# Kernel optimization log

Measured on AMD Instinct MI355X. Metric: run time of the kernel, lower is better.

Reference implementation:

```python
import jax, jax.numpy as jnp
import numpy as np

EPS = 1e-05
GROUPS = 8


def setup_inputs() -> dict:
    key = jax.random.key(0)
    k1, k2, k3 = jax.random.split(key, 3)
    N, C, H, W = 32, 256, 56, 56
    x = jax.random.normal(k1, (N, C, H, W), dtype=jnp.float32)
    weight = jnp.ones((C,), dtype=jnp.float32)
    bias = jnp.zeros((C,), dtype=jnp.float32)
    gate_logits = jnp.array([2.8, 0.2, 1.1], dtype=jnp.float32)
    diag_proj = jnp.array([[0.08, -0.05, 0.08],
                           [-0.03, 0.08, -0.01],
                           [-0.05, -0.04, -0.07]], dtype=jnp.float32)
    return {"x": x, "weight": weight, "bias": bias,
            "gate_logits": gate_logits, "diag_proj": diag_proj}


def reference(x, weight, bias, gate_logits, diag_proj):
    xf = x.astype(jnp.float32)
    N, C, H, W = xf.shape

    # variance descriptor (differentiable: first-instance path recomputes without detach)
    batch_var = jnp.var(xf, axis=(0, 2, 3)).mean()    # per-channel var -> mean
    sample_var = jnp.var(xf, axis=(1, 2, 3)).mean()   # per-sample var -> mean
    channel_var = jnp.var(xf, axis=1).mean()          # var over channels at each (n,h,w) -> mean
    desc = jnp.tanh(jnp.log(jnp.maximum(jnp.stack([batch_var, sample_var, channel_var]), EPS)))

    gate = jax.nn.softmax(gate_logits + diag_proj @ desc)  # [3]

    # batch norm (training mode: batch statistics over N,H,W per channel)
    mu_b = xf.mean(axis=(0, 2, 3), keepdims=True)
    var_b = xf.var(axis=(0, 2, 3), keepdims=True)
    x_bn = (xf - mu_b) / jnp.sqrt(var_b + EPS)

    # layer norm = group_norm with 1 group: per-sample stats over C,H,W
    mu_l = xf.mean(axis=(1, 2, 3), keepdims=True)
    var_l = xf.var(axis=(1, 2, 3), keepdims=True)
    x_ln = (xf - mu_l) / jnp.sqrt(var_l + EPS)

    # group norm with GROUPS groups
    xg = xf.reshape(N, GROUPS, C // GROUPS, H, W)
    mu_g = xg.mean(axis=(2, 3, 4), keepdims=True)
    var_g = xg.var(axis=(2, 3, 4), keepdims=True)
    x_gn = ((xg - mu_g) / jnp.sqrt(var_g + EPS)).reshape(N, C, H, W)

    mixed = gate[0] * x_bn + gate[1] * x_ln + gate[2] * x_gn
    y = mixed * weight[None, :, None, None] + bias[None, :, None, None]
    return y.astype(x.dtype)
```

## Files before the change

kernel.cpp:

```cpp
#include <hip/hip_runtime.h>
#include <hip/hip_bf16.h>

#define NN 32
#define CC 256
#define HW 3136
#define HW4 784
#define CHW 802816
#define CHW4 200704
#define NCHW 25690112
#define GROUPS 8
#define CPG 32
#define NHW 100352
#define GHW 100352
#define EPSF 1e-5f

#define PB16 49
#define NSTAT (NN*PB16)
#define NPT2 NSTAT

typedef float f32x4 __attribute__((ext_vector_type(4)));

__global__ __launch_bounds__(256) void stats_kernel(
    const float4* __restrict__ x4,
    float2* __restrict__ S12p,
    float* __restrict__ pT2)
{
    const int bx = blockIdx.x;
    const int n = bx / PB16, pb = bx - n * PB16;
    const int tid = threadIdx.x;
    const int w = tid >> 6, lane = tid & 63;
    const int cl = lane >> 3;
    const int pl = lane & 7;
    const int P0 = pb * 16;

    const float4* base = x4 + (size_t)n * CHW4 + P0 + pl;

    __shared__ float2 shS[256][9];
    __shared__ float4 shT[4][16];

    float s1a[8], s2a[8];
    float4 T0 = make_float4(0.f, 0.f, 0.f, 0.f);
    float4 T1 = make_float4(0.f, 0.f, 0.f, 0.f);
    #pragma unroll
    for (int k = 0; k < 8; ++k) {
        const int c = (k * 4 + w) * 8 + cl;
        float4 v0 = base[(size_t)c * HW4];
        float4 v1 = base[(size_t)c * HW4 + 8];
        T0.x += v0.x; T0.y += v0.y; T0.z += v0.z; T0.w += v0.w;
        T1.x += v1.x; T1.y += v1.y; T1.z += v1.z; T1.w += v1.w;
        s1a[k] = v0.x + v0.y + v0.z + v0.w + v1.x + v1.y + v1.z + v1.w;
        s2a[k] = v0.x*v0.x + v0.y*v0.y + v0.z*v0.z + v0.w*v0.w
               + v1.x*v1.x + v1.y*v1.y + v1.z*v1.z + v1.w*v1.w;
    }

    #pragma unroll
    for (int k = 0; k < 8; ++k) {
        const int c = (k * 4 + w) * 8 + cl;
        shS[c][pl] = make_float2(s1a[k], s2a[k]);
    }
    __syncthreads();

    {
        float a = 0.f, b = 0.f;
        #pragma unroll
        for (int j = 0; j < 8; ++j) {
            float2 v = shS[tid][j];
            a += v.x; b += v.y;
        }
        S12p[(size_t)bx * 256 + tid] = make_float2(a, b);
    }

    #pragma unroll
    for (int off = 8; off < 64; off <<= 1) {
        T0.x += __shfl_xor(T0.x, off, 64);
        T0.y += __shfl_xor(T0.y, off, 64);
        T0.z += __shfl_xor(T0.z, off, 64);
        T0.w += __shfl_xor(T0.w, off, 64);
        T1.x += __shfl_xor(T1.x, off, 64);
        T1.y += __shfl_xor(T1.y, off, 64);
        T1.z += __shfl_xor(T1.z, off, 64);
        T1.w += __shfl_xor(T1.w, off, 64);
    }
    if (lane < 8) {
        shT[w][pl] = T0;
        shT[w][8 + pl] = T1;
    }
    __syncthreads();
    if (tid < 16) {
        float4 a = shT[0][tid], b = shT[1][tid], c4 = shT[2][tid], d = shT[3][tid];
        const float tx = a.x + b.x + c4.x + d.x;
        const float ty = a.y + b.y + c4.y + d.y;
        const float tz = a.z + b.z + c4.z + d.z;
        const float tw = a.w + b.w + c4.w + d.w;
        float t2 = tx*tx + ty*ty + tz*tz + tw*tw;
        #pragma unroll
        for (int off = 1; off < 16; off <<= 1) t2 += __shfl_down(t2, off, 64);
        if (tid == 0) pT2[bx] = t2;
    }
}

__global__ __launch_bounds__(256) void fold_kernel(
    const float2* __restrict__ S12p, float2* __restrict__ S12)
{
    const int n = blockIdx.x, c = threadIdx.x;
    const float2* p = S12p + (size_t)n * PB16 * 256 + c;
    float a = 0.f, b = 0.f;
    #pragma unroll 7
    for (int pb = 0; pb < PB16; ++pb) {
        float2 v = p[(size_t)pb * 256];
        a += v.x; b += v.y;
    }
    S12[n * 256 + c] = make_float2(a, b);
}

__global__ __launch_bounds__(256) void finalize_kernel(
    const float2* __restrict__ S12, const float* __restrict__ partialT2,
    const float* __restrict__ gate_logits, const float* __restrict__ diag_proj,
    float2* __restrict__ CB, float2* __restrict__ CL, float2* __restrict__ CG,
    float* __restrict__ GT)
{
    const int tid = threadIdx.x;
    __shared__ float sh_red1[4], sh_red2[4], sh_red3[4], sh_red4[4];

    const float inv_NHW  = 1.f / (float)NHW;
    const float inv_CHW  = 1.f / (float)CHW;
    const float inv_GHW  = 1.f / (float)GHW;
    const float inv_NCHW = 1.f / (float)NCHW;

    const int c = tid;
    float s1 = 0.f, s2 = 0.f;
    for (int n = 0; n < NN; ++n) {
        float2 v = S12[n * CC + c];
        s1 += v.x; s2 += v.y;
    }
    const float mu_b  = s1 * inv_NHW;
    const float var_b = s2 * inv_NHW - mu_b * mu_b;
    CB[c] = make_float2(mu_b, rsqrtf(var_b + EPSF));

    const int ng_n = tid >> 3, ng_g = tid & 7;
    float s1g = 0.f, s2g = 0.f;
    for (int cc2 = 0; cc2 < CPG; ++cc2) {
        float2 v = S12[ng_n * CC + ng_g * CPG + cc2];
        s1g += v.x; s2g += v.y;
    }
    const float mu_g  = s1g * inv_GHW;
    const float var_g = s2g * inv_GHW - mu_g * mu_g;
    CG[tid] = make_float2(mu_g, rsqrtf(var_g + EPSF));

    float s1l = s1g, s2l = s2g;
    #pragma unroll
    for (int off = 1; off < 8; off <<= 1) {
        s1l += __shfl_xor(s1l, off, 64);
        s2l += __shfl_xor(s2l, off, 64);
    }
    float var_l_contrib = 0.f;
    if (ng_g == 0) {
        const float mu_l  = s1l * inv_CHW;
        const float var_l = s2l * inv_CHW - mu_l * mu_l;
        CL[ng_n] = make_float2(mu_l, rsqrtf(var_l + EPSF));
        var_l_contrib = var_l;
    }

    float t2p = 0.f;
    for (int i = tid; i < NPT2; i += 256) t2p += partialT2[i];

    float r1 = var_b, r2 = s2, r3 = var_l_contrib, r4 = t2p;
    #pragma unroll
    for (int off = 32; off; off >>= 1) {
        r1 += __shfl_down(r1, off, 64);
        r2 += __shfl_down(r2, off, 64);
        r3 += __shfl_down(r3, off, 64);
        r4 += __shfl_down(r4, off, 64);
    }
    const int wave = tid >> 6, lane = tid & 63;
    if (lane == 0) { sh_red1[wave] = r1; sh_red2[wave] = r2; sh_red3[wave] = r3; sh_red4[wave] = r4; }
    __syncthreads();
    if (tid == 0) {
        const float sum_var_b = sh_red1[0] + sh_red1[1] + sh_red1[2] + sh_red1[3];
        const float total_x2  = sh_red2[0] + sh_red2[1] + sh_red2[2] + sh_red2[3];
        const float sum_var_l = sh_red3[0] + sh_red3[1] + sh_red3[2] + sh_red3[3];
        const float sum_T2    = sh_red4[0] + sh_red4[1] + sh_red4[2] + sh_red4[3];

        const float batch_var   = sum_var_b * (1.f / (float)CC);
        const float sample_var  = sum_var_l * (1.f / (float)NN);
        const float channel_var = total_x2 * inv_NCHW
                                - sum_T2 * inv_NHW * (1.f / ((float)CC * (float)CC));

        float desc[3];
        desc[0] = tanhf(logf(fmaxf(batch_var,   EPSF)));
        desc[1] = tanhf(logf(fmaxf(sample_var,  EPSF)));
        desc[2] = tanhf(logf(fmaxf(channel_var, EPSF)));

        float lg[3];
        #pragma unroll
        for (int i = 0; i < 3; ++i) {
            lg[i] = gate_logits[i] + diag_proj[i*3+0]*desc[0]
                                   + diag_proj[i*3+1]*desc[1]
                                   + diag_proj[i*3+2]*desc[2];
        }
        const float m = fmaxf(lg[0], fmaxf(lg[1], lg[2]));
        const float e0 = expf(lg[0]-m), e1 = expf(lg[1]-m), e2 = expf(lg[2]-m);
        const float inv = 1.f / (e0 + e1 + e2);
        GT[0] = e0 * inv; GT[1] = e1 * inv; GT[2] = e2 * inv;
    }
}

__global__ __launch_bounds__(256) void apply_kernel(
    const f32x4* __restrict__ x4,
    const float* __restrict__ weight, const float* __restrict__ bias,
    const float2* __restrict__ CB, const float2* __restrict__ CL,
    const float2* __restrict__ CG, const float* __restrict__ GT,
    f32x4* __restrict__ y4)
{
    const int nc = blockIdx.x;
    const int n = nc >> 8, ch = nc & 255, g = ch >> 5;
    const float g0 = GT[0], g1 = GT[1], g2 = GT[2];
    const float2 cb = CB[ch], cl2 = CL[n], cg2 = CG[n * 8 + g];
    const float w = weight[ch], bi = bias[ch];
    const float scale = g0 * cb.y + g1 * cl2.y + g2 * cg2.y;
    const float offs  = g0 * cb.x * cb.y + g1 * cl2.x * cl2.y + g2 * cg2.x * cg2.y;
    const float a = w * scale;
    const float b = fmaf(-w, offs, bi);

    const f32x4* xp = x4 + (size_t)nc * HW4;
    f32x4* yp = y4 + (size_t)nc * HW4;
    const int tid = threadIdx.x;

    f32x4 v0 = xp[tid];
    f32x4 v1 = xp[tid + 256];
    f32x4 v2 = xp[tid + 512];
    f32x4 v3;
    if (tid < 16) v3 = xp[tid + 768];

    f32x4 r0, r1, r2, r3;
    r0.x = fmaf(v0.x, a, b); r0.y = fmaf(v0.y, a, b); r0.z = fmaf(v0.z, a, b); r0.w = fmaf(v0.w, a, b);
    r1.x = fmaf(v1.x, a, b); r1.y = fmaf(v1.y, a, b); r1.z = fmaf(v1.z, a, b); r1.w = fmaf(v1.w, a, b);
    r2.x = fmaf(v2.x, a, b); r2.y = fmaf(v2.y, a, b); r2.z = fmaf(v2.z, a, b); r2.w = fmaf(v2.w, a, b);
    __builtin_nontemporal_store(r0, &yp[tid]);
    __builtin_nontemporal_store(r1, &yp[tid + 256]);
    __builtin_nontemporal_store(r2, &yp[tid + 512]);
    if (tid < 16) {
        r3.x = fmaf(v3.x, a, b); r3.y = fmaf(v3.y, a, b); r3.z = fmaf(v3.z, a, b); r3.w = fmaf(v3.w, a, b);
        __builtin_nontemporal_store(r3, &yp[tid + 768]);
    }
}

extern "C" void kernel_launch(void* const* d_in, const int* in_sizes, int n_in,
                              void* d_out, int out_size, void* d_ws, size_t ws_size,
                              hipStream_t stream) {
    const float* x           = (const float*)d_in[0];
    const float* weight      = (const float*)d_in[1];
    const float* bias        = (const float*)d_in[2];
    const float* gate_logits = (const float*)d_in[3];
    const float* diag_proj   = (const float*)d_in[4];
    float* out = (float*)d_out;

    float* ws   = (float*)d_ws;
    float2* S12p = (float2*)ws;
    float2* S12  = (float2*)(ws + 802816);
    float2* CB   = (float2*)(ws + 819200);
    float2* CL   = (float2*)(ws + 819712);
    float2* CG   = (float2*)(ws + 819776);
    float*  GT   = ws + 820288;
    float*  pT2  = ws + 820296;

    stats_kernel<<<NSTAT, 256, 0, stream>>>((const float4*)x, S12p, pT2);
    fold_kernel<<<NN, 256, 0, stream>>>(S12p, S12);
    finalize_kernel<<<1, 256, 0, stream>>>(S12, pT2, gate_logits, diag_proj,
                                           CB, CL, CG, GT);
    apply_kernel<<<NN * CC, 256, 0, stream>>>((const f32x4*)x, weight, bias,
                                              CB, CL, CG, GT, (f32x4*)out);
}
```

Baseline: 62.97 us.

## Restructure stats pass into wide-pixel windows split across channel quarters

The stats kernel now gives each block a 64-float4 pixel window (13 windows per sample) and a quarter of the channels, instead of 16-pixel slices covering all channels. Each wavefront reads contiguous 1 KB rows per channel, and the per-channel partial sums are cut by about 4x, which shrinks the fold work and workspace. The cost is padded, predicated loads in the last window, more shared memory per block, and an extra cross-block partial for the channel-variance term. The apply kernel also switches from nontemporal stores to ordinary stores.

```diff
diff --git a/kernel.cpp b/kernel.cpp
--- a/kernel.cpp
+++ b/kernel.cpp
@@ -3,9 +3,7 @@
 
 #define NN 32
 #define CC 256
-#define HW 3136
 #define HW4 784
-#define CHW 802816
 #define CHW4 200704
 #define NCHW 25690112
 #define GROUPS 8
@@ -14,8 +12,8 @@
 #define GHW 100352
 #define EPSF 1e-5f
 
-#define PB16 49
-#define NSTAT (NN*PB16)
+#define WIN 13
+#define NSTAT (NN*WIN*4)
 #define NPT2 NSTAT
 
 typedef float f32x4 __attribute__((ext_vector_type(4)));
@@ -26,75 +24,59 @@
     float* __restrict__ pT2)
 {
     const int bx = blockIdx.x;
-    const int n = bx / PB16, pb = bx - n * PB16;
+    const int q   = bx & 3;
+    const int nw  = bx >> 2;
+    const int win = nw % WIN;
+    const int n   = nw / WIN;
     const int tid = threadIdx.x;
-    const int w = tid >> 6, lane = tid & 63;
-    const int cl = lane >> 3;
-    const int pl = lane & 7;
-    const int P0 = pb * 16;
-
-    const float4* base = x4 + (size_t)n * CHW4 + P0 + pl;
-
-    __shared__ float2 shS[256][9];
-    __shared__ float4 shT[4][16];
-
-    float s1a[8], s2a[8];
-    float4 T0 = make_float4(0.f, 0.f, 0.f, 0.f);
-    float4 T1 = make_float4(0.f, 0.f, 0.f, 0.f);
-    #pragma unroll
-    for (int k = 0; k < 8; ++k) {
-        const int c = (k * 4 + w) * 8 + cl;
-        float4 v0 = base[(size_t)c * HW4];
-        float4 v1 = base[(size_t)c * HW4 + 8];
-        T0.x += v0.x; T0.y += v0.y; T0.z += v0.z; T0.w += v0.w;
-        T1.x += v1.x; T1.y += v1.y; T1.z += v1.z; T1.w += v1.w;
-        s1a[k] = v0.x + v0.y + v0.z + v0.w + v1.x + v1.y + v1.z + v1.w;
-        s2a[k] = v0.x*v0.x + v0.y*v0.y + v0.z*v0.z + v0.w*v0.w
-               + v1.x*v1.x + v1.y*v1.y + v1.z*v1.z + v1.w*v1.w;
-    }
-
-    #pragma unroll
-    for (int k = 0; k < 8; ++k) {
-        const int c = (k * 4 + w) * 8 + cl;
-        shS[c][pl] = make_float2(s1a[k], s2a[k]);
-    }
+    const int w   = tid >> 6, lane = tid & 63;
+
+    const int p4 = win * 64 + lane;
+    const bool pv = p4 < HW4;
+    const int c0 = q * 64 + w * 16;
+
+    const float4* base = x4 + (size_t)n * CHW4 + p4;
+
+    __shared__ float sh1[64][65];
+    __shared__ float sh2[64][65];
+    __shared__ float4 shT[4][64];
+
+    float4 T = make_float4(0.f, 0.f, 0.f, 0.f);
+    #pragma unroll
+    for (int k = 0; k < 16; ++k) {
+        const int c = c0 + k;
+        float4 v = make_float4(0.f, 0.f, 0.f, 0.f);
+        if (pv) v = base[(size_t)c * HW4];
+        T.x += v.x; T.y += v.y; T.z += v.z; T.w += v.w;
+        sh1[w * 16 + k][lane] = v.x + v.y + v.z + v.w;
+        sh2[w * 16 + k][lane] = v.x*v.x + v.y*v.y + v.z*v.z + v.w*v.w;
+    }
+    shT[w][lane] = T;
     __syncthreads();
 
     {
+        const int cl = tid >> 2, seg = tid & 3;
         float a = 0.f, b = 0.f;
         #pragma unroll
-        for (int j = 0; j < 8; ++j) {
-            float2 v = shS[tid][j];
-            a += v.x; b += v.y;
+        for (int j = 0; j < 16; ++j) {
+            a += sh1[cl][seg * 16 + j];
+            b += sh2[cl][seg * 16 + j];
         }
-        S12p[(size_t)bx * 256 + tid] = make_float2(a, b);
-    }
-
-    #pragma unroll
-    for (int off = 8; off < 64; off <<= 1) {
-        T0.x += __shfl_xor(T0.x, off, 64);
-        T0.y += __shfl_xor(T0.y, off, 64);
-        T0.z += __shfl_xor(T0.z, off, 64);
-        T0.w += __shfl_xor(T0.w, off, 64);
-        T1.x += __shfl_xor(T1.x, off, 64);
-        T1.y += __shfl_xor(T1.y, off, 64);
-        T1.z += __shfl_xor(T1.z, off, 64);
-        T1.w += __shfl_xor(T1.w, off, 64);
-    }
-    if (lane < 8) {
-        shT[w][pl] = T0;
-        shT[w][8 + pl] = T1;
-    }
-    __syncthreads();
-    if (tid < 16) {
-        float4 a = shT[0][tid], b = shT[1][tid], c4 = shT[2][tid], d = shT[3][tid];
-        const float tx = a.x + b.x + c4.x + d.x;
-        const float ty = a.y + b.y + c4.y + d.y;
-        const float tz = a.z + b.z + c4.z + d.z;
-        const float tw = a.w + b.w + c4.w + d.w;
+        a += __shfl_down(a, 1, 64); b += __shfl_down(b, 1, 64);
+        a += __shfl_down(a, 2, 64); b += __shfl_down(b, 2, 64);
+        if (seg == 0)
+            S12p[(size_t)(n * WIN + win) * 256 + q * 64 + cl] = make_float2(a, b);
+    }
+
+    if (tid < 64) {
+        float4 a0 = shT[0][tid], a1 = shT[1][tid], a2 = shT[2][tid], a3 = shT[3][tid];
+        const float tx = a0.x + a1.x + a2.x + a3.x;
+        const float ty = a0.y + a1.y + a2.y + a3.y;
+        const float tz = a0.z + a1.z + a2.z + a3.z;
+        const float tw = a0.w + a1.w + a2.w + a3.w;
         float t2 = tx*tx + ty*ty + tz*tz + tw*tw;
         #pragma unroll
-        for (int off = 1; off < 16; off <<= 1) t2 += __shfl_down(t2, off, 64);
+        for (int off = 32; off; off >>= 1) t2 += __shfl_down(t2, off, 64);
         if (tid == 0) pT2[bx] = t2;
     }
 }
@@ -103,11 +85,11 @@
     const float2* __restrict__ S12p, float2* __restrict__ S12)
 {
     const int n = blockIdx.x, c = threadIdx.x;
-    const float2* p = S12p + (size_t)n * PB16 * 256 + c;
+    const float2* p = S12p + (size_t)n * WIN * 256 + c;
     float a = 0.f, b = 0.f;
-    #pragma unroll 7
-    for (int pb = 0; pb < PB16; ++pb) {
-        float2 v = p[(size_t)pb * 256];
+    #pragma unroll
+    for (int win = 0; win < WIN; ++win) {
+        float2 v = p[(size_t)win * 256];
         a += v.x; b += v.y;
     }
     S12[n * 256 + c] = make_float2(a, b);
@@ -123,7 +105,7 @@
     __shared__ float sh_red1[4], sh_red2[4], sh_red3[4], sh_red4[4];
 
     const float inv_NHW  = 1.f / (float)NHW;
-    const float inv_CHW  = 1.f / (float)CHW;
+    const float inv_CHW  = 1.f / (float)(CC * 3136);
     const float inv_GHW  = 1.f / (float)GHW;
     const float inv_NCHW = 1.f / (float)NCHW;
 
@@ -236,12 +218,12 @@
     r0.x = fmaf(v0.x, a, b); r0.y = fmaf(v0.y, a, b); r0.z = fmaf(v0.z, a, b); r0.w = fmaf(v0.w, a, b);
     r1.x = fmaf(v1.x, a, b); r1.y = fmaf(v1.y, a, b); r1.z = fmaf(v1.z, a, b); r1.w = fmaf(v1.w, a, b);
     r2.x = fmaf(v2.x, a, b); r2.y = fmaf(v2.y, a, b); r2.z = fmaf(v2.z, a, b); r2.w = fmaf(v2.w, a, b);
-    __builtin_nontemporal_store(r0, &yp[tid]);
-    __builtin_nontemporal_store(r1, &yp[tid + 256]);
-    __builtin_nontemporal_store(r2, &yp[tid + 512]);
+    yp[tid] = r0;
+    yp[tid + 256] = r1;
+    yp[tid + 512] = r2;
     if (tid < 16) {
         r3.x = fmaf(v3.x, a, b); r3.y = fmaf(v3.y, a, b); r3.z = fmaf(v3.z, a, b); r3.w = fmaf(v3.w, a, b);
-        __builtin_nontemporal_store(r3, &yp[tid + 768]);
+        yp[tid + 768] = r3;
     }
 }
 
@@ -255,14 +237,14 @@
     const float* diag_proj   = (const float*)d_in[4];
     float* out = (float*)d_out;
 
-    float* ws   = (float*)d_ws;
+    float* ws    = (float*)d_ws;
     float2* S12p = (float2*)ws;
-    float2* S12  = (float2*)(ws + 802816);
-    float2* CB   = (float2*)(ws + 819200);
-    float2* CL   = (float2*)(ws + 819712);
-    float2* CG   = (float2*)(ws + 819776);
-    float*  GT   = ws + 820288;
-    float*  pT2  = ws + 820296;
+    float2* S12  = (float2*)(ws + 212992);
+    float2* CB   = (float2*)(ws + 229376);
+    float2* CL   = (float2*)(ws + 229888);
+    float2* CG   = (float2*)(ws + 229952);
+    float*  GT   = ws + 230464;
+    float*  pT2  = ws + 230468;
 
     stats_kernel<<<NSTAT, 256, 0, stream>>>((const float4*)x, S12p, pT2);
     fold_kernel<<<NN, 256, 0, stream>>>(S12p, S12);
```

Result: no change. 62.79 us (-0.3%).
